# Optimization experiments

Hardware: AMD Instinct MI355X
Metric: run time of the kernel (lower is better)

Reference implementation:

```python
import jax, jax.numpy as jnp
import numpy as np

N, E = 50000, 640000
IN, HID, OUT, EDIM = 128, 128, 128, 3


def _linear(x, W, b):
    return x @ W + b


def setup_inputs() -> dict:
    key = jax.random.key(0)
    ks = jax.random.split(key, 16)
    s = lambda fi, fo: 1.0 / np.sqrt(fi)
    inp = {
        "x": jax.random.normal(ks[0], (N, IN), jnp.float32),
        "pos": jax.random.normal(ks[1], (N, 3), jnp.float32),
        "edge_index": jax.random.randint(ks[2], (2, E), 0, N, jnp.int32),
        "edge_attr": jax.random.normal(ks[3], (E, EDIM), jnp.float32),
        # message_mlp: Linear(2*IN+1+EDIM -> HID), SiLU, Linear(HID -> HID), SiLU
        "Wm1": jax.random.normal(ks[4], (2 * IN + 1 + EDIM, HID), jnp.float32) * s(2 * IN + 1 + EDIM, HID),
        "bm1": jnp.zeros((HID,), jnp.float32),
        "Wm2": jax.random.normal(ks[5], (HID, HID), jnp.float32) * s(HID, HID),
        "bm2": jnp.zeros((HID,), jnp.float32),
        # node_mlp: Linear(IN+HID -> HID), SiLU, Linear(HID -> OUT)
        "Wn1": jax.random.normal(ks[6], (IN + HID, HID), jnp.float32) * s(IN + HID, HID),
        "bn1": jnp.zeros((HID,), jnp.float32),
        "Wn2": jax.random.normal(ks[7], (HID, OUT), jnp.float32) * s(HID, OUT),
        "bn2": jnp.zeros((OUT,), jnp.float32),
        # coord_mlp: Linear(HID -> HID), SiLU, Linear(HID -> 1)
        "Wc1": jax.random.normal(ks[8], (HID, HID), jnp.float32) * s(HID, HID),
        "bc1": jnp.zeros((HID,), jnp.float32),
        "Wc2": jax.random.normal(ks[9], (HID, 1), jnp.float32) * s(HID, 1),
        "bc2": jnp.zeros((1,), jnp.float32),
    }
    return inp


def reference(x, pos, edge_index, edge_attr,
              Wm1, bm1, Wm2, bm2, Wn1, bn1, Wn2, bn2, Wc1, bc1, Wc2, bc2):
    row, col = edge_index[0], edge_index[1]
    diff = pos[row] - pos[col]                      # [E, 3]
    dist = jnp.linalg.norm(diff, axis=-1, keepdims=True)  # [E, 1]
    msg_input = jnp.concatenate([x[row], x[col], dist, edge_attr], axis=-1)
    h = jax.nn.silu(_linear(msg_input, Wm1, bm1))
    msg = jax.nn.silu(_linear(h, Wm2, bm2))        # [E, HID]
    agg = jax.ops.segment_sum(msg, row, num_segments=x.shape[0])  # [N, HID]
    hn = jax.nn.silu(_linear(jnp.concatenate([x, agg], axis=-1), Wn1, bn1))
    x_new = _linear(hn, Wn2, bn2)                  # [N, OUT]
    coord_w = _linear(jax.nn.silu(_linear(msg, Wc1, bc1)), Wc2, bc2)  # [E, 1]
    coord_agg = jax.ops.segment_sum(diff * coord_w, row, num_segments=pos.shape[0])
    pos_new = pos + coord_agg
    return (x_new, pos_new)
```

## Files before the change

kernel.cpp:

```cpp
#include <hip/hip_runtime.h>
#include <math.h>

#define NN 50000
#define NE 640000
#define HIDC 128
#define NTILES ((NN + 63)/64)

typedef short  short8 __attribute__((ext_vector_type(8)));
typedef __bf16 bf16x8 __attribute__((ext_vector_type(8)));
typedef float  f32x4  __attribute__((ext_vector_type(4)));
typedef unsigned int uint2v __attribute__((ext_vector_type(2)));
typedef unsigned int uint4v __attribute__((ext_vector_type(4)));

__device__ __forceinline__ unsigned short f2bf(float f) {
    unsigned int b = __float_as_uint(f);
    b += 0x7FFFu + ((b >> 16) & 1u);
    return (unsigned short)(b >> 16);
}
__device__ __forceinline__ float silu_f(float v) {
    return v * __builtin_amdgcn_rcpf(1.0f + __expf(-v));
}
__device__ __forceinline__ unsigned int cvtpk(float a, float b) {
    unsigned int r;
    asm("v_cvt_pk_bf16_f32 %0, %1, %2" : "=v"(r) : "v"(a), "v"(b));
    return r;
}

__global__ void conv_w_kernel(const float* __restrict__ Wm1, const float* __restrict__ Wm2,
                              const float* __restrict__ Wc1, const float* __restrict__ Wn1,
                              const float* __restrict__ Wn2,
                              unsigned short* __restrict__ wta, unsigned short* __restrict__ wtb,
                              unsigned short* __restrict__ wt2, unsigned short* __restrict__ wtc1,
                              unsigned short* __restrict__ wtn1, unsigned short* __restrict__ wtn2) {
    const int i = blockIdx.x * 256 + threadIdx.x;
    if (i < 16384) {
        const int n = i >> 7, k = i & 127;
        wta[i] = f2bf(Wm1[k * 128 + n]);
    } else if (i < 32768) {
        const int j = i - 16384; const int n = j >> 7, k = j & 127;
        wtb[j] = f2bf(Wm1[(128 + k) * 128 + n]);
    } else if (i < 49152) {
        const int j = i - 32768; const int n = j >> 7, k = j & 127;
        wt2[j] = f2bf(Wm2[k * 128 + n]);
    } else if (i < 65536) {
        const int j = i - 49152; const int n = j >> 7, k = j & 127;
        wtc1[j] = f2bf(Wc1[k * 128 + n]);
    } else if (i < 98304) {
        const int j = i - 65536; const int n = j >> 8, k = j & 255;
        wtn1[j] = f2bf(Wn1[k * 128 + n]);
    } else if (i < 114688) {
        const int j = i - 98304; const int n = j >> 7, k = j & 127;
        wtn2[j] = f2bf(Wn2[k * 128 + n]);
    }
}

__global__ void count_kernel(const int* __restrict__ ei, int* __restrict__ cnt) {
    const int e = blockIdx.x * 256 + threadIdx.x;
    if (e < NE) atomicAdd(&cnt[ei[e]], 1);
}

__global__ void scanA_kernel(const int* __restrict__ cnt, int* __restrict__ part) {
    __shared__ int ws[4];
    const int t = threadIdx.x, b = blockIdx.x;
    int v = (t < 200) ? cnt[b * 200 + t] : 0;
    #pragma unroll
    for (int d2 = 1; d2 < 64; d2 <<= 1) v += __shfl_xor(v, d2, 64);
    if ((t & 63) == 0) ws[t >> 6] = v;
    __syncthreads();
    if (t == 0) part[b] = ws[0] + ws[1] + ws[2] + ws[3];
}

__global__ void scanB_kernel(int* __restrict__ part) {
    const int t = threadIdx.x;
    int v[4]; int tot = 0;
    #pragma unroll
    for (int i = 0; i < 4; ++i) {
        const int idx = t * 4 + i;
        v[i] = (idx < 250) ? part[idx] : 0;
        tot += v[i];
    }
    int incl = tot;
    #pragma unroll
    for (int d2 = 1; d2 < 64; d2 <<= 1) { int u = __shfl_up(incl, d2, 64); if (t >= d2) incl += u; }
    int ex = incl - tot;
    #pragma unroll
    for (int i = 0; i < 4; ++i) {
        const int idx = t * 4 + i;
        if (idx < 250) part[idx] = ex;
        ex += v[i];
    }
}

__global__ void scanC_kernel(const int* __restrict__ cnt, const int* __restrict__ part,
                             int* __restrict__ offs2) {
    __shared__ int wex[4];
    const int t = threadIdx.x, b = blockIdx.x;
    const int lane = t & 63, w = t >> 6;
    int v = (t < 200) ? cnt[b * 200 + t] : 0;
    int incl = v;
    #pragma unroll
    for (int d2 = 1; d2 < 64; d2 <<= 1) { int u = __shfl_up(incl, d2, 64); if (lane >= d2) incl += u; }
    if (lane == 63) wex[w] = incl;
    __syncthreads();
    if (t == 0) { int a = 0; for (int i = 0; i < 4; ++i) { int x = wex[i]; wex[i] = a; a += x; } }
    __syncthreads();
    if (t < 200) offs2[b * 200 + t] = incl - v + wex[w] + part[b];
}

__global__ void scatter_kernel(const int* __restrict__ ei, const float* __restrict__ pos,
                               const float* __restrict__ eattr,
                               int* __restrict__ offs2, int4* __restrict__ epck) {
    const int e = blockIdx.x * 256 + threadIdx.x;
    if (e >= NE) return;
    const int s = ei[e], d = ei[NE + e];
    const int slot = atomicAdd(&offs2[s], 1);
    const float dx = pos[s*3+0] - pos[d*3+0];
    const float dy = pos[s*3+1] - pos[d*3+1];
    const float dz = pos[s*3+2] - pos[d*3+2];
    const float dist = sqrtf(dx*dx + dy*dy + dz*dz);
    int4 a, b;
    a.x = __float_as_int(dx); a.y = __float_as_int(dy);
    a.z = __float_as_int(dz); a.w = __float_as_int(dist);
    b.x = __float_as_int(eattr[e*3+0]); b.y = __float_as_int(eattr[e*3+1]);
    b.z = __float_as_int(eattr[e*3+2]); b.w = s | (d << 16);
    epck[(size_t)slot * 2 + 0] = a;
    epck[(size_t)slot * 2 + 1] = b;
}

__launch_bounds__(512, 4)
__global__ void pq_kernel(const float* __restrict__ x,
                          const unsigned short* __restrict__ wta,
                          const unsigned short* __restrict__ wtb,
                          const float* __restrict__ bm1v,
                          unsigned short* __restrict__ Pb, unsigned short* __restrict__ Qb)
{
    __shared__ __align__(16) unsigned short AN[64][128];
    const int tid = threadIdx.x;
    const int lane = tid & 63;
    const int wid = tid >> 6;
    const int lr = lane & 15;
    const int lg = lane >> 4;
    const int mycol = wid * 16 + lr;
    const float bm1_l = bm1v[mycol];
    const f32x4 z4 = {0.f, 0.f, 0.f, 0.f};
    const int n0 = blockIdx.x * 64;

    {
        const int i = tid >> 3, j = tid & 7;
        const int n = n0 + i;
        const bool ok = (n < NN);
        #pragma unroll
        for (int gi = 0; gi < 2; ++gi) {
            const int g = j + gi * 8;
            short8 v = {0,0,0,0,0,0,0,0};
            if (ok) {
                const float* xp = x + (size_t)n * HIDC + (g << 3);
                const f32x4 a = *reinterpret_cast<const f32x4*>(xp);
                const f32x4 b = *reinterpret_cast<const f32x4*>(xp + 4);
                #pragma unroll
                for (int cc = 0; cc < 4; ++cc) { v[cc] = (short)f2bf(a[cc]); v[cc+4] = (short)f2bf(b[cc]); }
            }
            *reinterpret_cast<short8*>(&AN[i][0] + ((g ^ (i & 7)) << 3)) = v;
        }
    }
    __syncthreads();

    f32x4 accp[4] = {z4, z4, z4, z4};
    f32x4 accq[4] = {z4, z4, z4, z4};
    #pragma unroll
    for (int kk = 0; kk < 4; ++kk) {
        const bf16x8 ba = *reinterpret_cast<const bf16x8*>(wta + mycol * 128 + kk * 32 + lg * 8);
        const bf16x8 bb = *reinterpret_cast<const bf16x8*>(wtb + mycol * 128 + kk * 32 + lg * 8);
        #pragma unroll
        for (int m = 0; m < 4; ++m) {
            const int r = m * 16 + lr;
            const bf16x8 a = *reinterpret_cast<const bf16x8*>(
                &AN[r][0] + (((kk * 4 + lg) ^ (r & 7)) << 3));
            accp[m] = __builtin_amdgcn_mfma_f32_16x16x32_bf16(a, ba, accp[m], 0, 0, 0);
            accq[m] = __builtin_amdgcn_mfma_f32_16x16x32_bf16(a, bb, accq[m], 0, 0, 0);
        }
    }
    #pragma unroll
    for (int m = 0; m < 4; ++m) {
        #pragma unroll
        for (int q = 0; q < 4; ++q) {
            const int n = n0 + m * 16 + lg * 4 + q;
            if (n < NN) {
                Pb[(size_t)n * HIDC + mycol] = f2bf(accp[m][q] + bm1_l);
                Qb[(size_t)n * HIDC + mycol] = f2bf(accq[m][q]);
            }
        }
    }
}

__launch_bounds__(1024, 4)
__global__ void edge_kernel(
    const unsigned short* __restrict__ Pb, const unsigned short* __restrict__ Qb,
    const int4* __restrict__ epck,
    const unsigned short* __restrict__ wt2g, const unsigned short* __restrict__ wtc1g,
    const float* __restrict__ Wm1,
    const float* __restrict__ bm2v, const float* __restrict__ bc1v,
    const float* __restrict__ wc2v, const float* __restrict__ bc2v,
    float* __restrict__ agg, float* __restrict__ cagg)
{
    __shared__ __align__(16) unsigned short wt2L[128][128];
    __shared__ __align__(16) unsigned short wtc1L[128][128];
    __shared__ __align__(16) float cons[4][128];
    __shared__ __align__(16) float w4F[128][4];
    __shared__ __align__(16) unsigned int MW[16][16 * 68];

    const int tid = threadIdx.x;
    const int lane = tid & 63;
    const int wid = tid >> 6;

    #pragma unroll
    for (int i = tid; i < 2048; i += 1024) {
        const int n = i >> 4, G = i & 15;
        *reinterpret_cast<short8*>(&wt2L[n][(G ^ (n & 7)) << 3]) =
            *reinterpret_cast<const short8*>(wt2g + n * 128 + G * 8);
    }
    #pragma unroll
    for (int i = tid; i < 2048; i += 1024) {
        const int n = i >> 4, G = i & 15;
        *reinterpret_cast<short8*>(&wtc1L[n][(G ^ (n & 7)) << 3]) =
            *reinterpret_cast<const short8*>(wtc1g + n * 128 + G * 8);
    }
    if (tid < 512) { const int h = tid >> 2, w = tid & 3; w4F[h][w] = Wm1[(256 + w) * 128 + h]; }
    if (tid < 384) {
        const int r = tid >> 7, j = tid & 127;
        cons[r][j] = (r == 0) ? bm2v[j] : (r == 1) ? bc1v[j] : wc2v[j];
    }
    __syncthreads();
    const float bc2s = bc2v[0];

    const int c = lane & 15, g = lane >> 4, c7 = c & 7;
    unsigned int* mw = &MW[wid][0];
    const f32x4 z4 = {0.f, 0.f, 0.f, 0.f};

    const int gw = blockIdx.x * 16 + wid;
    int t = gw * 10;
    const int tEnd = t + 10;

    int cur = -1; float s0a = 0.f, s1a = 0.f;

    auto flushA = [&]() {
        const float u1 = __shfl(s0a, lane >> 1, 64);
        const float v1 = __shfl(s1a, lane >> 1, 64);
        atomicAdd(&agg[(size_t)cur * HIDC + lane], (lane & 1) ? v1 : u1);
        const float u2 = __shfl(s0a, 32 + (lane >> 1), 64);
        const float v2 = __shfl(s1a, 32 + (lane >> 1), 64);
        atomicAdd(&agg[(size_t)cur * HIDC + 64 + lane], (lane & 1) ? v2 : u2);
    };

    int4 eA = epck[(size_t)(t * 16 + c) * 2 + 0];
    int4 eB = epck[(size_t)(t * 16 + c) * 2 + 1];

    bf16x8 Pf[4], Qf[4];
    {
        const int s0 = eB.w & 0xffff;
        const int d0 = ((unsigned)eB.w) >> 16;
        #pragma unroll
        for (int kk = 0; kk < 4; ++kk) {
            Pf[kk] = *reinterpret_cast<const bf16x8*>(Pb + (size_t)s0 * HIDC + kk * 32 + g * 8);
            Qf[kk] = *reinterpret_cast<const bf16x8*>(Qb + (size_t)d0 * HIDC + kk * 32 + g * 8);
        }
    }

    for (; t < tEnd; ++t) {
        const float dx = __int_as_float(eA.x);
        const float dy = __int_as_float(eA.y);
        const float dz = __int_as_float(eA.z);
        const float dist = __int_as_float(eA.w);
        const float ea0 = __int_as_float(eB.x);
        const float ea1 = __int_as_float(eB.y);
        const float ea2 = __int_as_float(eB.z);
        const int s = eB.w & 0xffff;
        const bool more = (t + 1 < tEnd);

        if (more) {
            eA = epck[(size_t)((t + 1) * 16 + c) * 2 + 0];
            eB = epck[(size_t)((t + 1) * 16 + c) * 2 + 1];
        }

        f32x4 acc2[8] = {z4, z4, z4, z4, z4, z4, z4, z4};
        #pragma unroll
        for (int kk = 0; kk < 4; ++kk) {
            const int hb = kk * 32 + g * 8;
            uint4v hw;
            #pragma unroll
            for (int jp = 0; jp < 4; ++jp) {
                float hv[2];
                #pragma unroll
                for (int u = 0; u < 2; ++u) {
                    const int j = 2 * jp + u;
                    const f32x4 w = *reinterpret_cast<const f32x4*>(&w4F[hb + j][0]);
                    const float hvv = (float)Pf[kk][j] + (float)Qf[kk][j]
                        + dist * w[0] + ea0 * w[1] + ea1 * w[2] + ea2 * w[3];
                    hv[u] = silu_f(hvv);
                }
                hw[jp] = cvtpk(hv[0], hv[1]);
            }
            const bf16x8 hf = *reinterpret_cast<const bf16x8*>(&hw);
            __builtin_amdgcn_s_setprio(1);
            #pragma unroll
            for (int mt = 0; mt < 8; ++mt) {
                const bf16x8 a = *reinterpret_cast<const bf16x8*>(
                    &wt2L[mt * 16 + c][(((kk << 2) + g) ^ c7) << 3]);
                acc2[mt] = __builtin_amdgcn_mfma_f32_16x16x32_bf16(a, hf, acc2[mt], 0, 0, 0);
            }
            __builtin_amdgcn_s_setprio(0);
        }

        if (more) {
            const int sN = eB.w & 0xffff;
            const int dN = ((unsigned)eB.w) >> 16;
            #pragma unroll
            for (int kk = 0; kk < 4; ++kk) {
                Pf[kk] = *reinterpret_cast<const bf16x8*>(Pb + (size_t)sN * HIDC + kk * 32 + g * 8);
                Qf[kk] = *reinterpret_cast<const bf16x8*>(Qb + (size_t)dN * HIDC + kk * 32 + g * 8);
            }
        }

        #pragma unroll
        for (int mt = 0; mt < 8; ++mt) {
            const f32x4 bm2q = *reinterpret_cast<const f32x4*>(&cons[0][mt * 16 + 4 * g]);
            const unsigned int p0 = cvtpk(silu_f(acc2[mt][0] + bm2q[0]), silu_f(acc2[mt][1] + bm2q[1]));
            const unsigned int p1 = cvtpk(silu_f(acc2[mt][2] + bm2q[2]), silu_f(acc2[mt][3] + bm2q[3]));
            *reinterpret_cast<uint2v*>(&mw[c * 68 + 8 * mt + 2 * g]) = (uint2v){p0, p1};
        }
        asm volatile("s_waitcnt lgkmcnt(0)" ::: "memory");
        __builtin_amdgcn_sched_barrier(0);

        f32x4 acc3[8] = {z4, z4, z4, z4, z4, z4, z4, z4};
        #pragma unroll
        for (int kk = 0; kk < 4; ++kk) {
            const bf16x8 bfr = *reinterpret_cast<const bf16x8*>(&mw[c * 68 + 16 * kk + 4 * g]);
            __builtin_amdgcn_s_setprio(1);
            #pragma unroll
            for (int mt = 0; mt < 8; ++mt) {
                const bf16x8 a = *reinterpret_cast<const bf16x8*>(
                    &wtc1L[mt * 16 + c][(((kk << 2) + g) ^ c7) << 3]);
                acc3[mt] = __builtin_amdgcn_mfma_f32_16x16x32_bf16(a, bfr, acc3[mt], 0, 0, 0);
            }
            __builtin_amdgcn_s_setprio(0);
        }

        float cw = 0.f;
        #pragma unroll
        for (int mt = 0; mt < 8; ++mt) {
            const f32x4 bc1q = *reinterpret_cast<const f32x4*>(&cons[1][mt * 16 + 4 * g]);
            const f32x4 wc2q = *reinterpret_cast<const f32x4*>(&cons[2][mt * 16 + 4 * g]);
            #pragma unroll
            for (int q = 0; q < 4; ++q)
                cw += silu_f(acc3[mt][q] + bc1q[q]) * wc2q[q];
        }
        cw += __shfl_xor(cw, 16, 64);
        cw += __shfl_xor(cw, 32, 64);
        cw += bc2s;

        float vx = dx * cw, vy = dy * cw, vz = dz * cw;
        #pragma unroll
        for (int dd = 1; dd < 16; dd <<= 1) {
            const int su = __shfl_up(s, dd, 16);
            const float ux = __shfl_up(vx, dd, 16);
            const float uy = __shfl_up(vy, dd, 16);
            const float uz = __shfl_up(vz, dd, 16);
            if (c >= dd && su == s) { vx += ux; vy += uy; vz += uz; }
        }
        {
            const int sdn = __shfl_down(s, 1, 16);
            if (g == 0 && (c == 15 || sdn != s)) {
                atomicAdd(&cagg[s * 3 + 0], vx);
                atomicAdd(&cagg[s * 3 + 1], vy);
                atomicAdd(&cagg[s * 3 + 2], vz);
            }
        }

        #pragma unroll
        for (int eh = 0; eh < 2; ++eh) {
            unsigned int rv8[8];
            #pragma unroll
            for (int e = 0; e < 8; ++e) rv8[e] = mw[(eh * 8 + e) * 68 + lane];
            #pragma unroll
            for (int e = 0; e < 8; ++e) {
                const int se = __builtin_amdgcn_readlane(s, eh * 8 + e);
                const float f0 = __uint_as_float(rv8[e] << 16);
                const float f1 = __uint_as_float(rv8[e] & 0xffff0000u);
                if (se != cur) {
                    if (cur >= 0) flushA();
                    cur = se; s0a = f0; s1a = f1;
                } else { s0a += f0; s1a += f1; }
            }
        }
    }
    if (cur >= 0) flushA();
}

__launch_bounds__(512, 4)
__global__ void node_kernel(
    const float* __restrict__ x, const float* __restrict__ agg,
    const float* __restrict__ cagg,
    const unsigned short* __restrict__ wtn1, const unsigned short* __restrict__ wtn2,
    const float* __restrict__ bn1v, const float* __restrict__ bn2v,
    const float* __restrict__ pos,
    float* __restrict__ outx, float* __restrict__ outp)
{
    __shared__ __align__(16) unsigned short AN[64][256];
    __shared__ __align__(16) unsigned short HN[64][HIDC];
    const int tid = threadIdx.x;
    const int lane = tid & 63;
    const int wid = tid >> 6;
    const int lr = lane & 15;
    const int lg = lane >> 4;
    const int mycol = wid * 16 + lr;
    const float bn1_l = bn1v[mycol];
    const float bn2_l = bn2v[mycol];
    const f32x4 z4 = {0.f, 0.f, 0.f, 0.f};
    const int n0 = blockIdx.x * 64;

    {
        const int i = tid >> 3, j = tid & 7;
        const int n = n0 + i;
        const bool ok = (n < NN);
        #pragma unroll
        for (int gi = 0; gi < 4; ++gi) {
            const int g = j + gi * 8;
            short8 v = {0,0,0,0,0,0,0,0};
            if (ok) {
                const float* sp = (g < 16) ? (x + (size_t)n * HIDC + (g << 3))
                                           : (agg + (size_t)n * HIDC + ((g - 16) << 3));
                const f32x4 a = *reinterpret_cast<const f32x4*>(sp);
                const f32x4 b = *reinterpret_cast<const f32x4*>(sp + 4);
                #pragma unroll
                for (int cc = 0; cc < 4; ++cc) { v[cc] = (short)f2bf(a[cc]); v[cc+4] = (short)f2bf(b[cc]); }
            }
            *reinterpret_cast<short8*>(&AN[i][0] + ((g ^ (i & 7)) << 3)) = v;
        }
    }
    __syncthreads();

    f32x4 acc[4] = {z4, z4, z4, z4};
    #pragma unroll
    for (int kk = 0; kk < 8; ++kk) {
        const bf16x8 b = *reinterpret_cast<const bf16x8*>(wtn1 + mycol * 256 + kk * 32 + lg * 8);
        #pragma unroll
        for (int m = 0; m < 4; ++m) {
            const int r = m * 16 + lr;
            const bf16x8 a = *reinterpret_cast<const bf16x8*>(
                &AN[r][0] + (((kk * 4 + lg) ^ (r & 7)) << 3));
            acc[m] = __builtin_amdgcn_mfma_f32_16x16x32_bf16(a, b, acc[m], 0, 0, 0);
        }
    }
    #pragma unroll
    for (int m = 0; m < 4; ++m) {
        #pragma unroll
        for (int q = 0; q < 4; ++q) {
            const int r = m * 16 + lg * 4 + q;
            HN[r][mycol ^ ((r & 7) << 3)] = f2bf(silu_f(acc[m][q] + bn1_l));
        }
    }
    __syncthreads();

    f32x4 acc2[4] = {z4, z4, z4, z4};
    #pragma unroll
    for (int kk = 0; kk < 4; ++kk) {
        const bf16x8 b = *reinterpret_cast<const bf16x8*>(wtn2 + mycol * 128 + kk * 32 + lg * 8);
        #pragma unroll
        for (int m = 0; m < 4; ++m) {
            const int r = m * 16 + lr;
            const bf16x8 a = *reinterpret_cast<const bf16x8*>(
                &HN[r][0] + (((kk * 4 + lg) ^ (r & 7)) << 3));
            acc2[m] = __builtin_amdgcn_mfma_f32_16x16x32_bf16(a, b, acc2[m], 0, 0, 0);
        }
    }
    #pragma unroll
    for (int m = 0; m < 4; ++m) {
        #pragma unroll
        for (int q = 0; q < 4; ++q) {
            const int n = n0 + m * 16 + lg * 4 + q;
            if (n < NN) outx[(size_t)n * HIDC + mycol] = acc2[m][q] + bn2_l;
        }
    }
    if (tid < 192) {
        const int r = n0 + tid / 3;
        const int d2 = tid - (tid / 3) * 3;
        if (r < NN) outp[r * 3 + d2] = pos[r * 3 + d2] + cagg[r * 3 + d2];
    }
}

extern "C" void kernel_launch(void* const* d_in, const int* in_sizes, int n_in,
                              void* d_out, int out_size, void* d_ws, size_t ws_size,
                              hipStream_t stream)
{
    const float* x   = (const float*)d_in[0];
    const float* pos = (const float*)d_in[1];
    const int*   ei  = (const int*)d_in[2];
    const float* ea  = (const float*)d_in[3];
    const float* Wm1 = (const float*)d_in[4];
    const float* bm1 = (const float*)d_in[5];
    const float* Wm2 = (const float*)d_in[6];
    const float* bm2 = (const float*)d_in[7];
    const float* Wn1 = (const float*)d_in[8];
    const float* bn1 = (const float*)d_in[9];
    const float* Wn2 = (const float*)d_in[10];
    const float* bn2 = (const float*)d_in[11];
    const float* Wc1 = (const float*)d_in[12];
    const float* bc1 = (const float*)d_in[13];
    const float* Wc2 = (const float*)d_in[14];
    const float* bc2 = (const float*)d_in[15];

    char* ws = (char*)d_ws;
    unsigned short* Pb   = (unsigned short*)(ws);
    unsigned short* Qb   = (unsigned short*)(ws + 12800000);
    float* agg           = (float*)(ws + 25600000);
    float* cagg          = (float*)(ws + 51200000);
    int*   cnt           = (int*)(ws + 51800000);
    int*   offs2         = (int*)(ws + 52000000);
    int*   part          = (int*)(ws + 52200000);
    int4*  epck          = (int4*)(ws + 52201024);
    unsigned short* wta  = (unsigned short*)(ws + 72681024);
    unsigned short* wtb  = (unsigned short*)(ws + 72713792);
    unsigned short* wt2  = (unsigned short*)(ws + 72746560);
    unsigned short* wtc1 = (unsigned short*)(ws + 72779328);
    unsigned short* wtn1 = (unsigned short*)(ws + 72812096);
    unsigned short* wtn2 = (unsigned short*)(ws + 72877632);

    float* outx = (float*)d_out;
    float* outp = outx + (size_t)NN * HIDC;

    conv_w_kernel<<<448, 256, 0, stream>>>(Wm1, Wm2, Wc1, Wn1, Wn2,
                                           wta, wtb, wt2, wtc1, wtn1, wtn2);
    hipMemsetAsync(cnt, 0, NN * sizeof(int), stream);
    count_kernel<<<2500, 256, 0, stream>>>(ei, cnt);
    scanA_kernel<<<250, 256, 0, stream>>>(cnt, part);
    scanB_kernel<<<1, 64, 0, stream>>>(part);
    scanC_kernel<<<250, 256, 0, stream>>>(cnt, part, offs2);
    scatter_kernel<<<2500, 256, 0, stream>>>(ei, pos, ea, offs2, epck);
    pq_kernel<<<NTILES, 512, 0, stream>>>(x, wta, wtb, bm1, Pb, Qb);
    hipMemsetAsync(agg, 0, (size_t)NN * HIDC * sizeof(float), stream);
    hipMemsetAsync(cagg, 0, (size_t)NN * 3 * sizeof(float), stream);
    edge_kernel<<<250, 1024, 0, stream>>>(Pb, Qb, epck, wt2, wtc1, Wm1,
                                          bm2, bc1, Wc2, bc2, agg, cagg);
    node_kernel<<<NTILES, 512, 0, stream>>>(x, agg, cagg, wtn1, wtn2, bn1, bn2,
                                            pos, outx, outp);
}
```

Measured before the change: 248.3 us.

## Fuse setup kernels, fold agg zeroing into pq kernel, rebalance edge grid

The weight-conversion kernel and the edge-count kernel become one launch, with extra blocks doing the counting. The three-stage scan is replaced by a single 1024-thread block scan. The agg/cagg memsets move into 200 extra blocks of pq_kernel, which zero the buffers with vector stores. The edge kernel now runs 256 blocks, with tiles split as 9 or 10 per warp. The aim is to cut launch count and idle gaps and to fill the GPU more evenly. The cost is that the single-block scan is serial and latency-bound, and the zeroing blocks compete with pq work.

```diff
diff --git a/kernel.cpp b/kernel.cpp
--- a/kernel.cpp
+++ b/kernel.cpp
@@ -26,12 +26,18 @@
     return r;
 }
 
-__global__ void conv_w_kernel(const float* __restrict__ Wm1, const float* __restrict__ Wm2,
-                              const float* __restrict__ Wc1, const float* __restrict__ Wn1,
-                              const float* __restrict__ Wn2,
-                              unsigned short* __restrict__ wta, unsigned short* __restrict__ wtb,
-                              unsigned short* __restrict__ wt2, unsigned short* __restrict__ wtc1,
-                              unsigned short* __restrict__ wtn1, unsigned short* __restrict__ wtn2) {
+__global__ void convw_count_kernel(const float* __restrict__ Wm1, const float* __restrict__ Wm2,
+                                   const float* __restrict__ Wc1, const float* __restrict__ Wn1,
+                                   const float* __restrict__ Wn2, const int* __restrict__ ei,
+                                   unsigned short* __restrict__ wta, unsigned short* __restrict__ wtb,
+                                   unsigned short* __restrict__ wt2, unsigned short* __restrict__ wtc1,
+                                   unsigned short* __restrict__ wtn1, unsigned short* __restrict__ wtn2,
+                                   int* __restrict__ cnt) {
+    if (blockIdx.x >= 448) {
+        const int e = (blockIdx.x - 448) * 256 + threadIdx.x;
+        if (e < NE) atomicAdd(&cnt[ei[e]], 1);
+        return;
+    }
     const int i = blockIdx.x * 256 + threadIdx.x;
     if (i < 16384) {
         const int n = i >> 7, k = i & 127;
@@ -54,57 +60,24 @@
     }
 }
 
-__global__ void count_kernel(const int* __restrict__ ei, int* __restrict__ cnt) {
-    const int e = blockIdx.x * 256 + threadIdx.x;
-    if (e < NE) atomicAdd(&cnt[ei[e]], 1);
-}
-
-__global__ void scanA_kernel(const int* __restrict__ cnt, int* __restrict__ part) {
-    __shared__ int ws[4];
-    const int t = threadIdx.x, b = blockIdx.x;
-    int v = (t < 200) ? cnt[b * 200 + t] : 0;
-    #pragma unroll
-    for (int d2 = 1; d2 < 64; d2 <<= 1) v += __shfl_xor(v, d2, 64);
-    if ((t & 63) == 0) ws[t >> 6] = v;
+__global__ void scan_fused_kernel(const int* __restrict__ cnt, int* __restrict__ offs2) {
+    __shared__ int wtot[16];
+    const int t = threadIdx.x, lane = t & 63, wid = t >> 6;
+    const int base = t * 49;
+    int s = 0;
+    for (int i = 0; i < 49; ++i) { const int idx = base + i; if (idx < NN) s += cnt[idx]; }
+    int inc = s;
+    #pragma unroll
+    for (int d = 1; d < 64; d <<= 1) { int u = __shfl_up(inc, d, 64); if (lane >= d) inc += u; }
+    if (lane == 63) wtot[wid] = inc;
     __syncthreads();
-    if (t == 0) part[b] = ws[0] + ws[1] + ws[2] + ws[3];
-}
-
-__global__ void scanB_kernel(int* __restrict__ part) {
-    const int t = threadIdx.x;
-    int v[4]; int tot = 0;
-    #pragma unroll
-    for (int i = 0; i < 4; ++i) {
-        const int idx = t * 4 + i;
-        v[i] = (idx < 250) ? part[idx] : 0;
-        tot += v[i];
-    }
-    int incl = tot;
-    #pragma unroll
-    for (int d2 = 1; d2 < 64; d2 <<= 1) { int u = __shfl_up(incl, d2, 64); if (t >= d2) incl += u; }
-    int ex = incl - tot;
-    #pragma unroll
-    for (int i = 0; i < 4; ++i) {
-        const int idx = t * 4 + i;
-        if (idx < 250) part[idx] = ex;
-        ex += v[i];
-    }
-}
-
-__global__ void scanC_kernel(const int* __restrict__ cnt, const int* __restrict__ part,
-                             int* __restrict__ offs2) {
-    __shared__ int wex[4];
-    const int t = threadIdx.x, b = blockIdx.x;
-    const int lane = t & 63, w = t >> 6;
-    int v = (t < 200) ? cnt[b * 200 + t] : 0;
-    int incl = v;
-    #pragma unroll
-    for (int d2 = 1; d2 < 64; d2 <<= 1) { int u = __shfl_up(incl, d2, 64); if (lane >= d2) incl += u; }
-    if (lane == 63) wex[w] = incl;
+    if (t == 0) { int a = 0; for (int w = 0; w < 16; ++w) { int v = wtot[w]; wtot[w] = a; a += v; } }
     __syncthreads();
-    if (t == 0) { int a = 0; for (int i = 0; i < 4; ++i) { int x = wex[i]; wex[i] = a; a += x; } }
-    __syncthreads();
-    if (t < 200) offs2[b * 200 + t] = incl - v + wex[w] + part[b];
+    int pre = wtot[wid] + inc - s;
+    for (int i = 0; i < 49; ++i) {
+        const int idx = base + i;
+        if (idx < NN) { offs2[idx] = pre; pre += cnt[idx]; }
+    }
 }
 
 __global__ void scatter_kernel(const int* __restrict__ ei, const float* __restrict__ pos,
@@ -132,8 +105,16 @@
                           const unsigned short* __restrict__ wta,
                           const unsigned short* __restrict__ wtb,
                           const float* __restrict__ bm1v,
-                          unsigned short* __restrict__ Pb, unsigned short* __restrict__ Qb)
+                          unsigned short* __restrict__ Pb, unsigned short* __restrict__ Qb,
+                          float* __restrict__ aggz)
 {
+    if (blockIdx.x >= NTILES) {
+        const int zt = (blockIdx.x - NTILES) * 512 + threadIdx.x;
+        const f32x4 z4v = {0.f, 0.f, 0.f, 0.f};
+        for (size_t i = zt; i < 1637500; i += 102400)
+            *reinterpret_cast<f32x4*>(aggz + i * 4) = z4v;
+        return;
+    }
     __shared__ __align__(16) unsigned short AN[64][128];
     const int tid = threadIdx.x;
     const int lane = tid & 63;
@@ -238,8 +219,8 @@
     const f32x4 z4 = {0.f, 0.f, 0.f, 0.f};
 
     const int gw = blockIdx.x * 16 + wid;
-    int t = gw * 10;
-    const int tEnd = t + 10;
+    int t = gw * 9 + (gw < 3136 ? gw : 3136);
+    const int tEnd = t + 9 + (gw < 3136 ? 1 : 0);
 
     int cur = -1; float s0a = 0.f, s1a = 0.f;
 
@@ -516,7 +497,6 @@
     float* cagg          = (float*)(ws + 51200000);
     int*   cnt           = (int*)(ws + 51800000);
     int*   offs2         = (int*)(ws + 52000000);
-    int*   part          = (int*)(ws + 52200000);
     int4*  epck          = (int4*)(ws + 52201024);
     unsigned short* wta  = (unsigned short*)(ws + 72681024);
     unsigned short* wtb  = (unsigned short*)(ws + 72713792);
@@ -528,18 +508,13 @@
     float* outx = (float*)d_out;
     float* outp = outx + (size_t)NN * HIDC;
 
-    conv_w_kernel<<<448, 256, 0, stream>>>(Wm1, Wm2, Wc1, Wn1, Wn2,
-                                           wta, wtb, wt2, wtc1, wtn1, wtn2);
     hipMemsetAsync(cnt, 0, NN * sizeof(int), stream);
-    count_kernel<<<2500, 256, 0, stream>>>(ei, cnt);
-    scanA_kernel<<<250, 256, 0, stream>>>(cnt, part);
-    scanB_kernel<<<1, 64, 0, stream>>>(part);
-    scanC_kernel<<<250, 256, 0, stream>>>(cnt, part, offs2);
+    convw_count_kernel<<<448 + 2500, 256, 0, stream>>>(Wm1, Wm2, Wc1, Wn1, Wn2, ei,
+                                                       wta, wtb, wt2, wtc1, wtn1, wtn2, cnt);
+    scan_fused_kernel<<<1, 1024, 0, stream>>>(cnt, offs2);
     scatter_kernel<<<2500, 256, 0, stream>>>(ei, pos, ea, offs2, epck);
-    pq_kernel<<<NTILES, 512, 0, stream>>>(x, wta, wtb, bm1, Pb, Qb);
-    hipMemsetAsync(agg, 0, (size_t)NN * HIDC * sizeof(float), stream);
-    hipMemsetAsync(cagg, 0, (size_t)NN * 3 * sizeof(float), stream);
-    edge_kernel<<<250, 1024, 0, stream>>>(Pb, Qb, epck, wt2, wtc1, Wm1,
+    pq_kernel<<<NTILES + 200, 512, 0, stream>>>(x, wta, wtb, bm1, Pb, Qb, agg);
+    edge_kernel<<<256, 1024, 0, stream>>>(Pb, Qb, epck, wt2, wtc1, Wm1,
                                           bm2, bc1, Wc2, bc2, agg, cagg);
     node_kernel<<<NTILES, 512, 0, stream>>>(x, agg, cagg, wtn1, wtn2, bn1, bn2,
                                             pos, outx, outp);
```

Result: slower. 323.1 us (+30.1%).

## Fuse weight conversion with edge counting, fold agg zeroing into pq, rebalance edges

Applied to the files above, without the earlier changes.

Weight conversion and edge-degree counting now run in one launch, with extra blocks taking the count work. Zeroing of the agg and cagg buffers moves from two memsets into extra blocks of pq_kernel, which relies on agg and cagg sitting next to each other in the workspace. The edge kernel grid grows from 250 to 256 blocks, and its 40000 tiles are split unevenly so each warp gets 9 or 10, spreading work over all CUs. An explicit LDS waitcnt and sched barrier before the coord MLP are dropped, leaving ordering of LDS accesses to the compiler and hardware.

```diff
diff --git a/kernel.cpp b/kernel.cpp
--- a/kernel.cpp
+++ b/kernel.cpp
@@ -26,12 +26,18 @@
     return r;
 }
 
-__global__ void conv_w_kernel(const float* __restrict__ Wm1, const float* __restrict__ Wm2,
-                              const float* __restrict__ Wc1, const float* __restrict__ Wn1,
-                              const float* __restrict__ Wn2,
-                              unsigned short* __restrict__ wta, unsigned short* __restrict__ wtb,
-                              unsigned short* __restrict__ wt2, unsigned short* __restrict__ wtc1,
-                              unsigned short* __restrict__ wtn1, unsigned short* __restrict__ wtn2) {
+__global__ void convw_count_kernel(const float* __restrict__ Wm1, const float* __restrict__ Wm2,
+                                   const float* __restrict__ Wc1, const float* __restrict__ Wn1,
+                                   const float* __restrict__ Wn2, const int* __restrict__ ei,
+                                   unsigned short* __restrict__ wta, unsigned short* __restrict__ wtb,
+                                   unsigned short* __restrict__ wt2, unsigned short* __restrict__ wtc1,
+                                   unsigned short* __restrict__ wtn1, unsigned short* __restrict__ wtn2,
+                                   int* __restrict__ cnt) {
+    if (blockIdx.x >= 448) {
+        const int e = (blockIdx.x - 448) * 256 + threadIdx.x;
+        if (e < NE) atomicAdd(&cnt[ei[e]], 1);
+        return;
+    }
     const int i = blockIdx.x * 256 + threadIdx.x;
     if (i < 16384) {
         const int n = i >> 7, k = i & 127;
@@ -54,11 +60,6 @@
     }
 }
 
-__global__ void count_kernel(const int* __restrict__ ei, int* __restrict__ cnt) {
-    const int e = blockIdx.x * 256 + threadIdx.x;
-    if (e < NE) atomicAdd(&cnt[ei[e]], 1);
-}
-
 __global__ void scanA_kernel(const int* __restrict__ cnt, int* __restrict__ part) {
     __shared__ int ws[4];
     const int t = threadIdx.x, b = blockIdx.x;
@@ -132,8 +133,16 @@
                           const unsigned short* __restrict__ wta,
                           const unsigned short* __restrict__ wtb,
                           const float* __restrict__ bm1v,
-                          unsigned short* __restrict__ Pb, unsigned short* __restrict__ Qb)
+                          unsigned short* __restrict__ Pb, unsigned short* __restrict__ Qb,
+                          float* __restrict__ aggz)
 {
+    if (blockIdx.x >= NTILES) {
+        const int zt = (blockIdx.x - NTILES) * 512 + threadIdx.x;
+        const f32x4 z4v = {0.f, 0.f, 0.f, 0.f};
+        for (size_t i = zt; i < 1637500; i += 102400)
+            *reinterpret_cast<f32x4*>(aggz + i * 4) = z4v;
+        return;
+    }
     __shared__ __align__(16) unsigned short AN[64][128];
     const int tid = threadIdx.x;
     const int lane = tid & 63;
@@ -238,8 +247,8 @@
     const f32x4 z4 = {0.f, 0.f, 0.f, 0.f};
 
     const int gw = blockIdx.x * 16 + wid;
-    int t = gw * 10;
-    const int tEnd = t + 10;
+    int t = gw * 9 + (gw < 3136 ? gw : 3136);
+    const int tEnd = t + 9 + (gw < 3136 ? 1 : 0);
 
     int cur = -1; float s0a = 0.f, s1a = 0.f;
 
@@ -328,8 +337,6 @@
             const unsigned int p1 = cvtpk(silu_f(acc2[mt][2] + bm2q[2]), silu_f(acc2[mt][3] + bm2q[3]));
             *reinterpret_cast<uint2v*>(&mw[c * 68 + 8 * mt + 2 * g]) = (uint2v){p0, p1};
         }
-        asm volatile("s_waitcnt lgkmcnt(0)" ::: "memory");
-        __builtin_amdgcn_sched_barrier(0);
 
         f32x4 acc3[8] = {z4, z4, z4, z4, z4, z4, z4, z4};
         #pragma unroll
@@ -528,18 +535,15 @@
     float* outx = (float*)d_out;
     float* outp = outx + (size_t)NN * HIDC;
 
-    conv_w_kernel<<<448, 256, 0, stream>>>(Wm1, Wm2, Wc1, Wn1, Wn2,
-                                           wta, wtb, wt2, wtc1, wtn1, wtn2);
     hipMemsetAsync(cnt, 0, NN * sizeof(int), stream);
-    count_kernel<<<2500, 256, 0, stream>>>(ei, cnt);
+    convw_count_kernel<<<448 + 2500, 256, 0, stream>>>(Wm1, Wm2, Wc1, Wn1, Wn2, ei,
+                                                       wta, wtb, wt2, wtc1, wtn1, wtn2, cnt);
     scanA_kernel<<<250, 256, 0, stream>>>(cnt, part);
     scanB_kernel<<<1, 64, 0, stream>>>(part);
     scanC_kernel<<<250, 256, 0, stream>>>(cnt, part, offs2);
     scatter_kernel<<<2500, 256, 0, stream>>>(ei, pos, ea, offs2, epck);
-    pq_kernel<<<NTILES, 512, 0, stream>>>(x, wta, wtb, bm1, Pb, Qb);
-    hipMemsetAsync(agg, 0, (size_t)NN * HIDC * sizeof(float), stream);
-    hipMemsetAsync(cagg, 0, (size_t)NN * 3 * sizeof(float), stream);
-    edge_kernel<<<250, 1024, 0, stream>>>(Pb, Qb, epck, wt2, wtc1, Wm1,
+    pq_kernel<<<NTILES + 200, 512, 0, stream>>>(x, wta, wtb, bm1, Pb, Qb, agg);
+    edge_kernel<<<256, 1024, 0, stream>>>(Pb, Qb, epck, wt2, wtc1, Wm1,
                                           bm2, bc1, Wc2, bc2, agg, cagg);
     node_kernel<<<NTILES, 512, 0, stream>>>(x, agg, cagg, wtn1, wtn2, bn1, bn2,
                                             pos, outx, outp);
```

After: 244.9 us. No clear change (-1.3%).
